# Kernel optimization log

Measured on AMD Instinct MI355X. Metric: run time of the kernel, lower is better.

Reference implementation:

```python
import jax, jax.numpy as jnp
import numpy as np
import math

H, SQK, SV, PQK, PV = 12, 16, 16, 4, 8
C1, C2 = 384, 128
B, N = 1, 768


def _rand_rot(key, shape):
    # random proper rotation matrices via QR of gaussian matrices
    m = jax.random.normal(key, shape + (3, 3), dtype=jnp.float32)
    q, r = jnp.linalg.qr(m)
    d = jnp.sign(jnp.diagonal(r, axis1=-2, axis2=-1))
    return q * d[..., None, :]


def setup_inputs() -> dict:
    key = jax.random.key(0)
    ks = jax.random.split(key, 16)
    s = 0.05
    return {
        'act': jax.random.normal(ks[0], (B, N, C1), dtype=jnp.float32),
        'act_2d': jax.random.normal(ks[1], (B, N, N, C2), dtype=jnp.float32),
        'sequence_mask': jnp.ones((B, N, 1), dtype=jnp.float32),
        'rot': _rand_rot(ks[2], (B, N)),
        'trans': jax.random.normal(ks[3], (B, N, 3), dtype=jnp.float32),
        'wq': jax.random.normal(ks[4], (C1, H * SQK), dtype=jnp.float32) * s,
        'wk': jax.random.normal(ks[5], (C1, H * SQK), dtype=jnp.float32) * s,
        'wv': jax.random.normal(ks[6], (C1, H * SV), dtype=jnp.float32) * s,
        'wqp': jax.random.normal(ks[7], (C1, H * PQK * 3), dtype=jnp.float32) * s,
        'bqp': jnp.zeros((H * PQK * 3,), dtype=jnp.float32),
        'wkp': jax.random.normal(ks[8], (C1, H * PQK * 3), dtype=jnp.float32) * s,
        'bkp': jnp.zeros((H * PQK * 3,), dtype=jnp.float32),
        'wvp': jax.random.normal(ks[9], (C1, H * PV * 3), dtype=jnp.float32) * s,
        'bvp': jnp.zeros((H * PV * 3,), dtype=jnp.float32),
        'w2d': jax.random.normal(ks[10], (C2, H), dtype=jnp.float32) * s,
        'b2d': jnp.zeros((H,), dtype=jnp.float32),
        'wfin': jax.random.normal(ks[11], (H * (C2 + SV + 4 * PV), C1), dtype=jnp.float32) * s,
        'bfin': jnp.zeros((C1,), dtype=jnp.float32),
        'tw': jnp.zeros((H,), dtype=jnp.float32),
    }


def _points(act, w, b, P):
    # torch: view [...,H,P*3] -> split into 3 chunks of P -> stack last => layout [H,3,P]
    p = (act @ w + b).reshape(*act.shape[:-1], H, 3, P)
    p = jnp.moveaxis(p, -2, -1)  # [B,N,H,P,3]
    return p.reshape(*act.shape[:-1], H * P, 3)


def _ipa(act, act_2d, sequence_mask, rot, trans,
         wq, wk, wv, wqp, bqp, wkp, bkp, wvp, bvp, w2d, b2d, wfin, bfin, tw):
    b, n, _ = act.shape
    q = (act @ wq).reshape(b, n, H, SQK) * math.sqrt(1.0 / SQK)
    k = (act @ wk).reshape(b, n, H, SQK)
    v = (act @ wv).reshape(b, n, H, SV)

    apply = lambda p: jnp.einsum('bnij,bnpj->bnpi', rot, p) + trans[:, :, None, :]
    qp = apply(_points(act, wqp, bqp, PQK))  # [B,N,H*PQK,3]
    kp = apply(_points(act, wkp, bkp, PQK))
    vp = apply(_points(act, wvp, bvp, PV))   # [B,N,H*PV,3]

    # point-distance logits
    pw = math.sqrt(2.0 / (9.0 * PQK)) * jax.nn.softplus(tw)  # [H]
    d2 = jnp.sum(jnp.square(qp[:, :, None] - kp[:, None]), -1)  # [B,N,N,H*PQK]
    d2 = d2.reshape(b, n, n, H, PQK).sum(-1)                    # [B,N,N,H]
    logits = -0.5 * pw * d2
    logits = logits + jnp.einsum('bqhc,bkhc->bqkh', q, k)
    logits = logits + act_2d @ w2d + b2d
    mask_2d = sequence_mask * jnp.swapaxes(sequence_mask, -1, -2)  # [B,N,N]
    logits = logits - 1e5 * (1.0 - mask_2d)[..., None]
    logits = logits * math.sqrt(1.0 / 3.0)
    attn = jax.nn.softmax(logits, axis=-2)  # over key residues

    res_scalar = jnp.einsum('bqkh,bkhc->bqhc', attn, v).reshape(b, n, H * SV)
    vp5 = vp.reshape(b, n, H, PV, 3)
    rpg = jnp.einsum('bqkh,bkhpd->bqhpd', attn, vp5).reshape(b, n, H * PV, 3)
    rpl = jnp.einsum('bnji,bnpj->bnpi', rot, rpg - trans[:, :, None, :])  # invert_apply
    norms = jnp.linalg.norm(rpl, axis=-1)
    r2d = jnp.einsum('bijh,bijc->bihc', attn, act_2d).reshape(b, n, H * C2)
    final = jnp.concatenate(
        [res_scalar, rpl[..., 0], rpl[..., 1], rpl[..., 2], norms, r2d], axis=-1)
    return final @ wfin + bfin


def reference(act, act_2d, sequence_mask, rot, trans,
              wq, wk, wv, wqp, bqp, wkp, bkp, wvp, bvp, w2d, b2d, wfin, bfin, tw):
    return _ipa(act, act_2d, sequence_mask, rot, trans,
                wq, wk, wv, wqp, bqp, wkp, bkp, wvp, bvp, w2d, b2d, wfin, bfin, tw)
```

## Files before the change

kernel.cpp:

```cpp
#include <hip/hip_runtime.h>
#include <math.h>

#define NH    12
#define NRES  768
#define C1V   384
#define C2V   128
#define NPROJ 1152
#define QKD   28
#define FDIM  2112
#define VVD   480
#define APAD  772
#define KSPLIT 11

typedef __attribute__((ext_vector_type(8))) short bf16x8;
typedef __attribute__((ext_vector_type(4))) float f32x4;

__device__ __forceinline__ float softplusf_(float x) {
    return (x > 20.f) ? x : log1pf(__expf(x));
}
__device__ __forceinline__ ushort f2bf(float x) {
    union { float f; unsigned u; } v; v.f = x;
    unsigned r = (v.u + 0x7fffu + ((v.u >> 16) & 1u)) >> 16;
    return (ushort)r;
}

__global__ __launch_bounds__(256) void kW_prep(
    const float* __restrict__ w2d, ushort* __restrict__ w2dT)
{
    int idx = blockIdx.x * 256 + threadIdx.x;
    int h = idx >> 7, c = idx & 127;
    w2dT[idx] = (h < NH) ? f2bf(w2d[c * NH + h]) : (ushort)0;
}

__global__ __launch_bounds__(256) void k1_proj(
    const float* __restrict__ act,
    const float* __restrict__ wq, const float* __restrict__ wk,
    const float* __restrict__ wv, const float* __restrict__ wqp,
    const float* __restrict__ wkp, const float* __restrict__ wvp,
    const float* __restrict__ bqp, const float* __restrict__ bkp,
    const float* __restrict__ bvp, float* __restrict__ proj)
{
    __shared__ float As[64 * 33];
    __shared__ float Bs[32 * 65];
    const int n0 = blockIdx.x * 64, m0 = blockIdx.y * 64;
    const int tid = threadIdx.x;
    const int tx = tid & 15, ty = tid >> 4;
    float c[4][4] = {};

    for (int kt = 0; kt < C1V; kt += 32) {
        for (int idx = tid; idx < 64 * 32; idx += 256) {
            int r = idx >> 5, j = idx & 31;
            As[r * 33 + j] = act[(m0 + r) * C1V + kt + j];
        }
        for (int idx = tid; idx < 32 * 64; idx += 256) {
            int r = idx >> 6, col = idx & 63;
            int jj = n0 + col, k = kt + r;
            float w;
            if      (jj < 192) w = wq [k * 192 + jj];
            else if (jj < 384) w = wk [k * 192 + jj - 192];
            else if (jj < 576) w = wv [k * 192 + jj - 384];
            else if (jj < 720) w = wqp[k * 144 + jj - 576];
            else if (jj < 864) w = wkp[k * 144 + jj - 720];
            else               w = wvp[k * 288 + jj - 864];
            Bs[r * 65 + col] = w;
        }
        __syncthreads();
        #pragma unroll
        for (int kk = 0; kk < 32; ++kk) {
            float a[4], b[4];
            #pragma unroll
            for (int i = 0; i < 4; ++i) a[i] = As[(ty * 4 + i) * 33 + kk];
            #pragma unroll
            for (int j = 0; j < 4; ++j) b[j] = Bs[kk * 65 + tx * 4 + j];
            #pragma unroll
            for (int i = 0; i < 4; ++i)
                #pragma unroll
                for (int j = 0; j < 4; ++j) c[i][j] += a[i] * b[j];
        }
        __syncthreads();
    }
    float biasv[4];
    #pragma unroll
    for (int j = 0; j < 4; ++j) {
        int col = n0 + tx * 4 + j;
        biasv[j] = (col >= 864) ? bvp[col - 864]
                 : (col >= 720) ? bkp[col - 720]
                 : (col >= 576) ? bqp[col - 576] : 0.f;
    }
    #pragma unroll
    for (int i = 0; i < 4; ++i) {
        float4 v;
        v.x = c[i][0] + biasv[0]; v.y = c[i][1] + biasv[1];
        v.z = c[i][2] + biasv[2]; v.w = c[i][3] + biasv[3];
        *(float4*)&proj[(m0 + ty * 4 + i) * NPROJ + n0 + tx * 4] = v;
    }
}

__global__ __launch_bounds__(64) void k2_prep(
    const float* __restrict__ proj, const float* __restrict__ rot,
    const float* __restrict__ trans, const float* __restrict__ tw,
    float* __restrict__ Qv, float* __restrict__ Kv,
    float* __restrict__ akArr, float* __restrict__ vv)
{
    const int n = blockIdx.x, tid = threadIdx.x;
    __shared__ float kp2[48];
    const float* pr = proj + n * NPROJ;
    float R[9], T[3];
    #pragma unroll
    for (int i = 0; i < 9; ++i) R[i] = rot[n * 9 + i];
    #pragma unroll
    for (int i = 0; i < 3; ++i) T[i] = trans[n * 3 + i];

    for (int idx = tid; idx < 192; idx += 64) {
        int h = idx >> 4, cc = idx & 15;
        Qv[(n * NH + h) * QKD + cc] = pr[idx] * 0.25f;
        Kv[(n * NH + h) * QKD + cc] = pr[192 + idx];
        vv[n * VVD + idx] = pr[384 + idx];
    }
    if (tid < 48) {
        int h = tid >> 2, p = tid & 3;
        float pwh = 0.23570226039551584f * softplusf_(tw[h]);
        float lx = pr[576 + h * 12 + p];
        float ly = pr[576 + h * 12 + 4 + p];
        float lz = pr[576 + h * 12 + 8 + p];
        float gx = R[0] * lx + R[1] * ly + R[2] * lz + T[0];
        float gy = R[3] * lx + R[4] * ly + R[5] * lz + T[1];
        float gz = R[6] * lx + R[7] * ly + R[8] * lz + T[2];
        float* qd = &Qv[(n * NH + h) * QKD + 16];
        qd[p] = pwh * gx; qd[4 + p] = pwh * gy; qd[8 + p] = pwh * gz;
        lx = pr[720 + h * 12 + p];
        ly = pr[720 + h * 12 + 4 + p];
        lz = pr[720 + h * 12 + 8 + p];
        gx = R[0] * lx + R[1] * ly + R[2] * lz + T[0];
        gy = R[3] * lx + R[4] * ly + R[5] * lz + T[1];
        gz = R[6] * lx + R[7] * ly + R[8] * lz + T[2];
        float* kd = &Kv[(n * NH + h) * QKD + 16];
        kd[p] = gx; kd[4 + p] = gy; kd[8 + p] = gz;
        kp2[tid] = gx * gx + gy * gy + gz * gz;
    }
    __syncthreads();
    if (tid < NH) {
        float pwh = 0.23570226039551584f * softplusf_(tw[tid]);
        akArr[n * NH + tid] = -0.5f * pwh *
            (kp2[tid * 4] + kp2[tid * 4 + 1] + kp2[tid * 4 + 2] + kp2[tid * 4 + 3]);
    }
    for (int idx = tid; idx < 96; idx += 64) {
        int h = idx >> 3, p = idx & 7;
        float lx = pr[864 + h * 24 + p];
        float ly = pr[864 + h * 24 + 8 + p];
        float lz = pr[864 + h * 24 + 16 + p];
        float gx = R[0] * lx + R[1] * ly + R[2] * lz + T[0];
        float gy = R[3] * lx + R[4] * ly + R[5] * lz + T[1];
        float gz = R[6] * lx + R[7] * ly + R[8] * lz + T[2];
        float* dst = &vv[n * VVD + 192 + h * 24 + p * 3];
        dst[0] = gx; dst[1] = gy; dst[2] = gz;
    }
}

__global__ __launch_bounds__(256) void k2b_qk(
    const float* __restrict__ Qv, const float* __restrict__ Kv,
    const float* __restrict__ akArr, float* __restrict__ qkBuf)
{
    const int h = blockIdx.z;
    const int k0 = blockIdx.x * 64, q0 = blockIdx.y * 64;
    __shared__ float As[64 * 29];
    __shared__ float Bs[64 * 29];
    const int tid = threadIdx.x, tx = tid & 15, ty = tid >> 4;

    for (int idx = tid; idx < 64 * 28; idx += 256) {
        int r = idx / 28, j = idx - r * 28;
        As[r * 29 + j] = Qv[((q0 + r) * NH + h) * QKD + j];
        Bs[r * 29 + j] = Kv[((k0 + r) * NH + h) * QKD + j];
    }
    __syncthreads();
    float c[4][4] = {};
    #pragma unroll
    for (int kk = 0; kk < 28; ++kk) {
        float a[4], b[4];
        #pragma unroll
        for (int i = 0; i < 4; ++i) a[i] = As[(ty * 4 + i) * 29 + kk];
        #pragma unroll
        for (int j = 0; j < 4; ++j) b[j] = Bs[(tx * 4 + j) * 29 + kk];
        #pragma unroll
        for (int i = 0; i < 4; ++i)
            #pragma unroll
            for (int j = 0; j < 4; ++j) c[i][j] += a[i] * b[j];
    }
    float akv[4];
    #pragma unroll
    for (int j = 0; j < 4; ++j) akv[j] = akArr[(k0 + tx * 4 + j) * NH + h];
    #pragma unroll
    for (int i = 0; i < 4; ++i) {
        float4 v;
        v.x = c[i][0] + akv[0]; v.y = c[i][1] + akv[1];
        v.z = c[i][2] + akv[2]; v.w = c[i][3] + akv[3];
        *(float4*)&qkBuf[((q0 + ty * 4 + i) * NH + h) * NRES + k0 + tx * 4] = v;
    }
}

__global__ __launch_bounds__(256) void kA_mfma(
    const float* __restrict__ act2d, const float* __restrict__ smask,
    const ushort* __restrict__ w2dT, float* __restrict__ qkBuf)
{
    const int q = blockIdx.y, k0 = blockIdx.x * 64, tid = threadIdx.x;
    __shared__ ushort tile[64 * 136];
    const int lane = tid & 63, wv = tid >> 6;
    const int nb = lane & 15, quad = lane >> 4;

    bf16x8 bfr[4];
    #pragma unroll
    for (int s = 0; s < 4; ++s)
        bfr[s] = *(const bf16x8*)&w2dT[nb * 128 + quad * 8 + s * 32];

    const float* src = act2d + ((size_t)q * NRES + k0) * C2V;
    #pragma unroll
    for (int i = 0; i < 8; ++i) {
        int f = tid + i * 256;
        int r = f >> 5, c4 = f & 31;
        float4 v = ((const float4*)src)[f];
        ushort4 o = { f2bf(v.x), f2bf(v.y), f2bf(v.z), f2bf(v.w) };
        *(ushort4*)&tile[r * 136 + c4 * 4] = o;
    }
    __syncthreads();

    f32x4 acc = {0.f, 0.f, 0.f, 0.f};
    #pragma unroll
    for (int s = 0; s < 4; ++s) {
        bf16x8 af = *(const bf16x8*)&tile[(wv * 16 + nb) * 136 + quad * 8 + s * 32];
        acc = __builtin_amdgcn_mfma_f32_16x16x32_bf16(af, bfr[s], acc, 0, 0, 0);
    }

    if (nb < NH) {
        const int kb = k0 + wv * 16 + quad * 4;
        float* dst = &qkBuf[((size_t)(q * NH + nb)) * NRES + kb];
        float4 old = *(float4*)dst;
        float4 sm = *(const float4*)&smask[kb];
        const float smq = smask[q];
        const float scale = 0.5773502691896258f;
        float4 outv;
        outv.x = (old.x + acc[0] - 1e5f * (1.f - smq * sm.x)) * scale;
        outv.y = (old.y + acc[1] - 1e5f * (1.f - smq * sm.y)) * scale;
        outv.z = (old.z + acc[2] - 1e5f * (1.f - smq * sm.z)) * scale;
        outv.w = (old.w + acc[3] - 1e5f * (1.f - smq * sm.w)) * scale;
        *(float4*)dst = outv;
    }
}

__global__ __launch_bounds__(256) void kC_attn(
    const float* __restrict__ act2d, const float* __restrict__ qkBuf,
    const float* __restrict__ vv, const float* __restrict__ rot,
    const float* __restrict__ trans, float* __restrict__ F)
{
    const int q = blockIdx.x, tid = threadIdx.x;
    __shared__ float attnS[NH * APAD];
    __shared__ float scr[1536];
    __shared__ float red[NH * 4];
    __shared__ float mh[NH], lh[NH];
    __shared__ float rotS[9], transS[3];

    if (tid < 9) rotS[tid] = rot[q * 9 + tid];
    if (tid < 3) transS[tid] = trans[q * 3 + tid];

    float lg[3][NH];
    #pragma unroll
    for (int h = 0; h < NH; ++h)
        #pragma unroll
        for (int i = 0; i < 3; ++i)
            lg[i][h] = qkBuf[((size_t)(q * NH + h)) * NRES + tid + 256 * i];

    const int wv_ = tid >> 6, lane = tid & 63;
    #pragma unroll
    for (int h = 0; h < NH; ++h) {
        float v = fmaxf(fmaxf(lg[0][h], lg[1][h]), lg[2][h]);
        for (int off = 32; off > 0; off >>= 1) v = fmaxf(v, __shfl_down(v, off, 64));
        if (lane == 0) red[h * 4 + wv_] = v;
    }
    __syncthreads();
    if (tid < NH)
        mh[tid] = fmaxf(fmaxf(red[tid * 4], red[tid * 4 + 1]),
                        fmaxf(red[tid * 4 + 2], red[tid * 4 + 3]));
    __syncthreads();
    float lsum[NH];
    #pragma unroll
    for (int h = 0; h < NH; ++h) lsum[h] = 0.f;
    #pragma unroll
    for (int i = 0; i < 3; ++i)
        #pragma unroll
        for (int h = 0; h < NH; ++h) {
            float e = __expf(lg[i][h] - mh[h]);
            attnS[h * APAD + tid + 256 * i] = e;
            lsum[h] += e;
        }
    #pragma unroll
    for (int h = 0; h < NH; ++h) {
        float v = lsum[h];
        for (int off = 32; off > 0; off >>= 1) v += __shfl_down(v, off, 64);
        if (lane == 0) red[h * 4 + wv_] = v;
    }
    __syncthreads();
    if (tid < NH)
        lh[tid] = 1.f / (red[tid * 4] + red[tid * 4 + 1] + red[tid * 4 + 2] + red[tid * 4 + 3]);
    __syncthreads();

    const int cq = tid & 31, hg = (tid >> 5) & 3, kg = tid >> 7;
    const int h0 = 3 * hg;
    const float* abase = act2d + ((size_t)q * NRES + kg * 384) * C2V + cq * 4;
    const float* at0 = &attnS[(h0    ) * APAD + kg * 384];
    const float* at1 = &attnS[(h0 + 1) * APAD + kg * 384];
    const float* at2 = &attnS[(h0 + 2) * APAD + kg * 384];
    float4 a0 = {0,0,0,0}, a1 = {0,0,0,0}, a2 = {0,0,0,0};

    for (int kk = 0; kk < 384; kk += 4) {
        float4 t0 = *(const float4*)&abase[(size_t)(kk    ) * C2V];
        float4 t1 = *(const float4*)&abase[(size_t)(kk + 1) * C2V];
        float4 t2 = *(const float4*)&abase[(size_t)(kk + 2) * C2V];
        float4 t3 = *(const float4*)&abase[(size_t)(kk + 3) * C2V];
        float4 p0 = *(const float4*)&at0[kk];
        float4 p1 = *(const float4*)&at1[kk];
        float4 p2 = *(const float4*)&at2[kk];
        a0.x += p0.x*t0.x + p0.y*t1.x + p0.z*t2.x + p0.w*t3.x;
        a0.y += p0.x*t0.y + p0.y*t1.y + p0.z*t2.y + p0.w*t3.y;
        a0.z += p0.x*t0.z + p0.y*t1.z + p0.z*t2.z + p0.w*t3.z;
        a0.w += p0.x*t0.w + p0.y*t1.w + p0.z*t2.w + p0.w*t3.w;
        a1.x += p1.x*t0.x + p1.y*t1.x + p1.z*t2.x + p1.w*t3.x;
        a1.y += p1.x*t0.y + p1.y*t1.y + p1.z*t2.y + p1.w*t3.y;
        a1.z += p1.x*t0.z + p1.y*t1.z + p1.z*t2.z + p1.w*t3.z;
        a1.w += p1.x*t0.w + p1.y*t1.w + p1.z*t2.w + p1.w*t3.w;
        a2.x += p2.x*t0.x + p2.y*t1.x + p2.z*t2.x + p2.w*t3.x;
        a2.y += p2.x*t0.y + p2.y*t1.y + p2.z*t2.y + p2.w*t3.y;
        a2.z += p2.x*t0.z + p2.y*t1.z + p2.z*t2.z + p2.w*t3.z;
        a2.w += p2.x*t0.w + p2.y*t1.w + p2.z*t2.w + p2.w*t3.w;
    }
    if (kg == 1) {
        *(float4*)&scr[(h0    ) * 128 + cq * 4] = a0;
        *(float4*)&scr[(h0 + 1) * 128 + cq * 4] = a1;
        *(float4*)&scr[(h0 + 2) * 128 + cq * 4] = a2;
    }
    __syncthreads();
    float* Fq = F + q * FDIM;
    if (kg == 0) {
        float4 b0 = *(const float4*)&scr[(h0    ) * 128 + cq * 4];
        float4 b1 = *(const float4*)&scr[(h0 + 1) * 128 + cq * 4];
        float4 b2 = *(const float4*)&scr[(h0 + 2) * 128 + cq * 4];
        float l0 = lh[h0], l1 = lh[h0 + 1], l2 = lh[h0 + 2];
        float4 o0 = {(a0.x+b0.x)*l0, (a0.y+b0.y)*l0, (a0.z+b0.z)*l0, (a0.w+b0.w)*l0};
        float4 o1 = {(a1.x+b1.x)*l1, (a1.y+b1.y)*l1, (a1.z+b1.z)*l1, (a1.w+b1.w)*l1};
        float4 o2 = {(a2.x+b2.x)*l2, (a2.y+b2.y)*l2, (a2.z+b2.z)*l2, (a2.w+b2.w)*l2};
        *(float4*)&Fq[576 + (h0    ) * 128 + cq * 4] = o0;
        *(float4*)&Fq[576 + (h0 + 1) * 128 + cq * 4] = o1;
        *(float4*)&Fq[576 + (h0 + 2) * 128 + cq * 4] = o2;
    }
    __syncthreads();

    const int j4 = tid & 127;
    const int kgv = tid >> 7;
    float p0 = 0.f, p1 = 0.f, p2 = 0.f, p3 = 0.f;
    if (j4 < 120) {
        const int h = (j4 < 48) ? (j4 >> 2) : ((j4 - 48) / 6);
        const float* at = &attnS[h * APAD + kgv * 384];
        const float* col = vv + (size_t)(kgv * 384) * VVD + j4 * 4;
        #pragma unroll 4
        for (int k = 0; k < 384; ++k) {
            float a = at[k];
            float4 v = *(const float4*)(col + (size_t)k * VVD);
            p0 += a * v.x; p1 += a * v.y; p2 += a * v.z; p3 += a * v.w;
        }
    }
    __syncthreads();
    if (j4 < 120) {
        float4 pv = {p0, p1, p2, p3};
        *(float4*)&scr[(kgv * 120 + j4) * 4] = pv;
    }
    __syncthreads();
    if (tid < 120) {
        float4 a = *(const float4*)&scr[tid * 4];
        float4 b = *(const float4*)&scr[(120 + tid) * 4];
        const int h = (tid < 48) ? (tid >> 2) : ((tid - 48) / 6);
        const float il = lh[h];
        float4 s = {(a.x + b.x) * il, (a.y + b.y) * il,
                    (a.z + b.z) * il, (a.w + b.w) * il};
        if (tid < 48) {
            *(float4*)&Fq[tid * 4] = s;
        } else {
            *(float4*)&scr[1024 + (tid - 48) * 4] = s;
        }
    }
    __syncthreads();
    if (tid < 96) {
        float gx = scr[1024 + tid * 3]     - transS[0];
        float gy = scr[1024 + tid * 3 + 1] - transS[1];
        float gz = scr[1024 + tid * 3 + 2] - transS[2];
        float x = rotS[0] * gx + rotS[3] * gy + rotS[6] * gz;
        float y = rotS[1] * gx + rotS[4] * gy + rotS[7] * gz;
        float z = rotS[2] * gx + rotS[5] * gy + rotS[8] * gz;
        Fq[192 + tid] = x;
        Fq[288 + tid] = y;
        Fq[384 + tid] = z;
        Fq[480 + tid] = sqrtf(x * x + y * y + z * z);
    }
}

__global__ __launch_bounds__(256) void k5_partial(
    const float* __restrict__ F, const float* __restrict__ wfin,
    float* __restrict__ part)
{
    const int n0 = blockIdx.x * 64, m0 = blockIdx.y * 64, kz = blockIdx.z;
    const int kbeg = kz * 192;
    __shared__ float As[64 * 33];
    __shared__ float Bs[32 * 65];
    const int tid = threadIdx.x, tx = tid & 15, ty = tid >> 4;
    float c[4][4] = {};

    for (int kt = kbeg; kt < kbeg + 192; kt += 32) {
        for (int idx = tid; idx < 64 * 32; idx += 256) {
            int r = idx >> 5, j = idx & 31;
            As[r * 33 + j] = F[(m0 + r) * FDIM + kt + j];
        }
        for (int idx = tid; idx < 32 * 64; idx += 256) {
            int r = idx >> 6, col = idx & 63;
            Bs[r * 65 + col] = wfin[(kt + r) * 384 + n0 + col];
        }
        __syncthreads();
        #pragma unroll
        for (int kk = 0; kk < 32; ++kk) {
            float a[4], b[4];
            #pragma unroll
            for (int i = 0; i < 4; ++i) a[i] = As[(ty * 4 + i) * 33 + kk];
            #pragma unroll
            for (int j = 0; j < 4; ++j) b[j] = Bs[kk * 65 + tx * 4 + j];
            #pragma unroll
            for (int i = 0; i < 4; ++i)
                #pragma unroll
                for (int j = 0; j < 4; ++j) c[i][j] += a[i] * b[j];
        }
        __syncthreads();
    }
    float* dst = part + (size_t)kz * (768 * 384);
    #pragma unroll
    for (int i = 0; i < 4; ++i) {
        float4 v = {c[i][0], c[i][1], c[i][2], c[i][3]};
        *(float4*)&dst[(m0 + ty * 4 + i) * 384 + n0 + tx * 4] = v;
    }
}

__global__ __launch_bounds__(256) void k5_reduce(
    const float* __restrict__ part, const float* __restrict__ bfin,
    float* __restrict__ out)
{
    const int e = blockIdx.x * 256 + threadIdx.x;
    const float4* p = (const float4*)part;
    float4 b = ((const float4*)bfin)[e % 96];
    float4 s = {b.x, b.y, b.z, b.w};
    #pragma unroll
    for (int kz = 0; kz < KSPLIT; ++kz) {
        float4 v = p[(size_t)kz * 73728 + e];
        s.x += v.x; s.y += v.y; s.z += v.z; s.w += v.w;
    }
    ((float4*)out)[e] = s;
}

extern "C" void kernel_launch(void* const* d_in, const int* in_sizes, int n_in,
                              void* d_out, int out_size, void* d_ws, size_t ws_size,
                              hipStream_t stream) {
    const float* act   = (const float*)d_in[0];
    const float* act2d = (const float*)d_in[1];
    const float* smask = (const float*)d_in[2];
    const float* rot   = (const float*)d_in[3];
    const float* trans = (const float*)d_in[4];
    const float* wq    = (const float*)d_in[5];
    const float* wk    = (const float*)d_in[6];
    const float* wvv   = (const float*)d_in[7];
    const float* wqp   = (const float*)d_in[8];
    const float* bqp   = (const float*)d_in[9];
    const float* wkp   = (const float*)d_in[10];
    const float* bkp   = (const float*)d_in[11];
    const float* wvp   = (const float*)d_in[12];
    const float* bvp   = (const float*)d_in[13];
    const float* w2d   = (const float*)d_in[14];
    const float* wfin  = (const float*)d_in[16];
    const float* bfin  = (const float*)d_in[17];
    const float* tw    = (const float*)d_in[18];

    float* W     = (float*)d_ws;
    float* proj  = W;
    float* Qv    = proj  + 768 * NPROJ;
    float* Kv    = Qv    + 768 * NH * QKD;
    float* akArr = Kv    + 768 * NH * QKD;
    float* vvA   = akArr + 768 * NH;
    float* qkBuf = vvA   + 768 * VVD;
    float* F     = qkBuf + 768 * NH * NRES;
    ushort* w2dT = (ushort*)(F + 768 * FDIM);
    float* part  = qkBuf;

    kW_prep<<<dim3(8), 256, 0, stream>>>(w2d, w2dT);
    k1_proj<<<dim3(18, 12), 256, 0, stream>>>(act, wq, wk, wvv, wqp, wkp, wvp,
                                              bqp, bkp, bvp, proj);
    k2_prep<<<dim3(NRES), 64, 0, stream>>>(proj, rot, trans, tw, Qv, Kv, akArr, vvA);
    k2b_qk<<<dim3(12, 12, NH), 256, 0, stream>>>(Qv, Kv, akArr, qkBuf);
    kA_mfma<<<dim3(12, NRES), 256, 0, stream>>>(act2d, smask, w2dT, qkBuf);
    kC_attn<<<dim3(NRES), 256, 0, stream>>>(act2d, qkBuf, vvA, rot, trans, F);
    k5_partial<<<dim3(6, 12, KSPLIT), 256, 0, stream>>>(F, wfin, part);
    k5_reduce<<<dim3(288), 256, 0, stream>>>(part, bfin, (float*)d_out);
}
```

Before: 687.2 us.

## Fuse pair-bias MFMA and attention into one online-softmax kernel

Merges the kernel that computes the act_2d pair-bias logits with the attention kernel, using a flash-style online softmax over 64-key chunks. The goal is to stop reading the 300MB act_2d tensor twice and to avoid the qkBuf read-modify-write round trip. Each chunk's act_2d tile is loaded for the MFMA and then read again, likely from cache, for the weighted sum. The cost is one block per query with many barriers per chunk, so the kernel has much less parallelism than the 12x768 grid it replaces.

```diff
diff --git a/kernel.cpp b/kernel.cpp
--- a/kernel.cpp
+++ b/kernel.cpp
@@ -9,7 +9,6 @@
 #define QKD   28
 #define FDIM  2112
 #define VVD   480
-#define APAD  772
 #define KSPLIT 11
 
 typedef __attribute__((ext_vector_type(8))) short bf16x8;
@@ -198,139 +197,148 @@
     }
 }
 
-__global__ __launch_bounds__(256) void kA_mfma(
-    const float* __restrict__ act2d, const float* __restrict__ smask,
-    const ushort* __restrict__ w2dT, float* __restrict__ qkBuf)
-{
-    const int q = blockIdx.y, k0 = blockIdx.x * 64, tid = threadIdx.x;
+__global__ __launch_bounds__(256) void kF_fused(
+    const float* __restrict__ act2d, const float* __restrict__ qkBuf,
+    const float* __restrict__ smask, const ushort* __restrict__ w2dT,
+    const float* __restrict__ vv, const float* __restrict__ rot,
+    const float* __restrict__ trans, float* __restrict__ F)
+{
+    const int q = blockIdx.x, tid = threadIdx.x;
     __shared__ ushort tile[64 * 136];
-    const int lane = tid & 63, wv = tid >> 6;
+    __shared__ float p_lds[16 * 72];
+    __shared__ float redM[64], redS[64];
+    __shared__ float mS[16], sS[16], fS[16];
+    __shared__ float scr[1536];
+    __shared__ float rotS[9], transS[3];
+
+    const int lane = tid & 63, wvI = tid >> 6;
     const int nb = lane & 15, quad = lane >> 4;
+    const int cq = tid & 31, hg = (tid >> 5) & 3, kg = tid >> 7;
+    const int h0 = 3 * hg;
+    const int j4 = tid & 127, kgv = tid >> 7;
+    const int hv = (j4 < 48) ? (j4 >> 2) : ((j4 - 48) / 6);
 
     bf16x8 bfr[4];
     #pragma unroll
     for (int s = 0; s < 4; ++s)
         bfr[s] = *(const bf16x8*)&w2dT[nb * 128 + quad * 8 + s * 32];
 
-    const float* src = act2d + ((size_t)q * NRES + k0) * C2V;
-    #pragma unroll
-    for (int i = 0; i < 8; ++i) {
-        int f = tid + i * 256;
-        int r = f >> 5, c4 = f & 31;
-        float4 v = ((const float4*)src)[f];
-        ushort4 o = { f2bf(v.x), f2bf(v.y), f2bf(v.z), f2bf(v.w) };
-        *(ushort4*)&tile[r * 136 + c4 * 4] = o;
-    }
-    __syncthreads();
-
-    f32x4 acc = {0.f, 0.f, 0.f, 0.f};
-    #pragma unroll
-    for (int s = 0; s < 4; ++s) {
-        bf16x8 af = *(const bf16x8*)&tile[(wv * 16 + nb) * 136 + quad * 8 + s * 32];
-        acc = __builtin_amdgcn_mfma_f32_16x16x32_bf16(af, bfr[s], acc, 0, 0, 0);
-    }
-
-    if (nb < NH) {
-        const int kb = k0 + wv * 16 + quad * 4;
-        float* dst = &qkBuf[((size_t)(q * NH + nb)) * NRES + kb];
-        float4 old = *(float4*)dst;
-        float4 sm = *(const float4*)&smask[kb];
-        const float smq = smask[q];
-        const float scale = 0.5773502691896258f;
-        float4 outv;
-        outv.x = (old.x + acc[0] - 1e5f * (1.f - smq * sm.x)) * scale;
-        outv.y = (old.y + acc[1] - 1e5f * (1.f - smq * sm.y)) * scale;
-        outv.z = (old.z + acc[2] - 1e5f * (1.f - smq * sm.z)) * scale;
-        outv.w = (old.w + acc[3] - 1e5f * (1.f - smq * sm.w)) * scale;
-        *(float4*)dst = outv;
-    }
-}
-
-__global__ __launch_bounds__(256) void kC_attn(
-    const float* __restrict__ act2d, const float* __restrict__ qkBuf,
-    const float* __restrict__ vv, const float* __restrict__ rot,
-    const float* __restrict__ trans, float* __restrict__ F)
-{
-    const int q = blockIdx.x, tid = threadIdx.x;
-    __shared__ float attnS[NH * APAD];
-    __shared__ float scr[1536];
-    __shared__ float red[NH * 4];
-    __shared__ float mh[NH], lh[NH];
-    __shared__ float rotS[9], transS[3];
-
+    if (tid < 16) { mS[tid] = -1e30f; sS[tid] = 0.f; fS[tid] = 0.f; }
     if (tid < 9) rotS[tid] = rot[q * 9 + tid];
     if (tid < 3) transS[tid] = trans[q * 3 + tid];
-
-    float lg[3][NH];
-    #pragma unroll
-    for (int h = 0; h < NH; ++h)
-        #pragma unroll
-        for (int i = 0; i < 3; ++i)
-            lg[i][h] = qkBuf[((size_t)(q * NH + h)) * NRES + tid + 256 * i];
-
-    const int wv_ = tid >> 6, lane = tid & 63;
-    #pragma unroll
-    for (int h = 0; h < NH; ++h) {
-        float v = fmaxf(fmaxf(lg[0][h], lg[1][h]), lg[2][h]);
-        for (int off = 32; off > 0; off >>= 1) v = fmaxf(v, __shfl_down(v, off, 64));
-        if (lane == 0) red[h * 4 + wv_] = v;
-    }
-    __syncthreads();
-    if (tid < NH)
-        mh[tid] = fmaxf(fmaxf(red[tid * 4], red[tid * 4 + 1]),
-                        fmaxf(red[tid * 4 + 2], red[tid * 4 + 3]));
-    __syncthreads();
-    float lsum[NH];
-    #pragma unroll
-    for (int h = 0; h < NH; ++h) lsum[h] = 0.f;
-    #pragma unroll
-    for (int i = 0; i < 3; ++i)
-        #pragma unroll
-        for (int h = 0; h < NH; ++h) {
-            float e = __expf(lg[i][h] - mh[h]);
-            attnS[h * APAD + tid + 256 * i] = e;
-            lsum[h] += e;
-        }
-    #pragma unroll
-    for (int h = 0; h < NH; ++h) {
-        float v = lsum[h];
-        for (int off = 32; off > 0; off >>= 1) v += __shfl_down(v, off, 64);
-        if (lane == 0) red[h * 4 + wv_] = v;
-    }
-    __syncthreads();
-    if (tid < NH)
-        lh[tid] = 1.f / (red[tid * 4] + red[tid * 4 + 1] + red[tid * 4 + 2] + red[tid * 4 + 3]);
-    __syncthreads();
-
-    const int cq = tid & 31, hg = (tid >> 5) & 3, kg = tid >> 7;
-    const int h0 = 3 * hg;
-    const float* abase = act2d + ((size_t)q * NRES + kg * 384) * C2V + cq * 4;
-    const float* at0 = &attnS[(h0    ) * APAD + kg * 384];
-    const float* at1 = &attnS[(h0 + 1) * APAD + kg * 384];
-    const float* at2 = &attnS[(h0 + 2) * APAD + kg * 384];
+    const float smq = smask[q];
+
     float4 a0 = {0,0,0,0}, a1 = {0,0,0,0}, a2 = {0,0,0,0};
-
-    for (int kk = 0; kk < 384; kk += 4) {
-        float4 t0 = *(const float4*)&abase[(size_t)(kk    ) * C2V];
-        float4 t1 = *(const float4*)&abase[(size_t)(kk + 1) * C2V];
-        float4 t2 = *(const float4*)&abase[(size_t)(kk + 2) * C2V];
-        float4 t3 = *(const float4*)&abase[(size_t)(kk + 3) * C2V];
-        float4 p0 = *(const float4*)&at0[kk];
-        float4 p1 = *(const float4*)&at1[kk];
-        float4 p2 = *(const float4*)&at2[kk];
-        a0.x += p0.x*t0.x + p0.y*t1.x + p0.z*t2.x + p0.w*t3.x;
-        a0.y += p0.x*t0.y + p0.y*t1.y + p0.z*t2.y + p0.w*t3.y;
-        a0.z += p0.x*t0.z + p0.y*t1.z + p0.z*t2.z + p0.w*t3.z;
-        a0.w += p0.x*t0.w + p0.y*t1.w + p0.z*t2.w + p0.w*t3.w;
-        a1.x += p1.x*t0.x + p1.y*t1.x + p1.z*t2.x + p1.w*t3.x;
-        a1.y += p1.x*t0.y + p1.y*t1.y + p1.z*t2.y + p1.w*t3.y;
-        a1.z += p1.x*t0.z + p1.y*t1.z + p1.z*t2.z + p1.w*t3.z;
-        a1.w += p1.x*t0.w + p1.y*t1.w + p1.z*t2.w + p1.w*t3.w;
-        a2.x += p2.x*t0.x + p2.y*t1.x + p2.z*t2.x + p2.w*t3.x;
-        a2.y += p2.x*t0.y + p2.y*t1.y + p2.z*t2.y + p2.w*t3.y;
-        a2.z += p2.x*t0.z + p2.y*t1.z + p2.z*t2.z + p2.w*t3.z;
-        a2.w += p2.x*t0.w + p2.y*t1.w + p2.z*t2.w + p2.w*t3.w;
-    }
+    float v0 = 0.f, v1 = 0.f, v2 = 0.f, v3 = 0.f;
+
+    for (int kc = 0; kc < 12; ++kc) {
+        const int kbase = kc * 64;
+        const float* src = act2d + ((size_t)q * NRES + kbase) * C2V;
+        #pragma unroll
+        for (int i = 0; i < 8; ++i) {
+            int f = tid + i * 256;
+            int r = f >> 5, c4 = f & 31;
+            float4 v = ((const float4*)src)[f];
+            ushort4 o = { f2bf(v.x), f2bf(v.y), f2bf(v.z), f2bf(v.w) };
+            *(ushort4*)&tile[r * 136 + c4 * 4] = o;
+        }
+        const int kb = kbase + wvI * 16 + quad * 4;
+        float4 qk = {0,0,0,0}, mk = {1.f,1.f,1.f,1.f};
+        if (nb < NH) {
+            qk = *(const float4*)&qkBuf[((size_t)(q * NH + nb)) * NRES + kb];
+            mk = *(const float4*)&smask[kb];
+        }
+        __syncthreads();
+        f32x4 acc = {0.f, 0.f, 0.f, 0.f};
+        #pragma unroll
+        for (int s = 0; s < 4; ++s) {
+            bf16x8 af = *(const bf16x8*)&tile[(wvI * 16 + nb) * 136 + quad * 8 + s * 32];
+            acc = __builtin_amdgcn_mfma_f32_16x16x32_bf16(af, bfr[s], acc, 0, 0, 0);
+        }
+        float l0 = -1e30f, l1 = -1e30f, l2 = -1e30f, l3 = -1e30f;
+        if (nb < NH) {
+            const float scale = 0.5773502691896258f;
+            l0 = (qk.x + acc[0] - 1e5f * (1.f - smq * mk.x)) * scale;
+            l1 = (qk.y + acc[1] - 1e5f * (1.f - smq * mk.y)) * scale;
+            l2 = (qk.z + acc[2] - 1e5f * (1.f - smq * mk.z)) * scale;
+            l3 = (qk.w + acc[3] - 1e5f * (1.f - smq * mk.w)) * scale;
+        }
+        float lmax = fmaxf(fmaxf(l0, l1), fmaxf(l2, l3));
+        lmax = fmaxf(lmax, __shfl_xor(lmax, 16, 64));
+        lmax = fmaxf(lmax, __shfl_xor(lmax, 32, 64));
+        if (quad == 0) redM[nb * 4 + wvI] = lmax;
+        __syncthreads();
+        if (tid < NH) {
+            float cm = fmaxf(fmaxf(redM[tid * 4], redM[tid * 4 + 1]),
+                             fmaxf(redM[tid * 4 + 2], redM[tid * 4 + 3]));
+            float mo = mS[tid], mn = fmaxf(mo, cm);
+            fS[tid] = __expf(mo - mn);
+            mS[tid] = mn;
+        }
+        __syncthreads();
+        float psum = 0.f;
+        if (nb < NH) {
+            float mn = mS[nb];
+            float e0 = __expf(l0 - mn), e1 = __expf(l1 - mn);
+            float e2 = __expf(l2 - mn), e3 = __expf(l3 - mn);
+            psum = e0 + e1 + e2 + e3;
+            float4 ev = {e0, e1, e2, e3};
+            *(float4*)&p_lds[nb * 72 + wvI * 16 + quad * 4] = ev;
+        }
+        psum += __shfl_xor(psum, 16, 64);
+        psum += __shfl_xor(psum, 32, 64);
+        if (quad == 0) redS[nb * 4 + wvI] = psum;
+        __syncthreads();
+        if (tid < NH)
+            sS[tid] = sS[tid] * fS[tid] + redS[tid * 4] + redS[tid * 4 + 1]
+                                        + redS[tid * 4 + 2] + redS[tid * 4 + 3];
+        {
+            float f0 = fS[h0], f1 = fS[h0 + 1], f2 = fS[h0 + 2];
+            a0.x *= f0; a0.y *= f0; a0.z *= f0; a0.w *= f0;
+            a1.x *= f1; a1.y *= f1; a1.z *= f1; a1.w *= f1;
+            a2.x *= f2; a2.y *= f2; a2.z *= f2; a2.w *= f2;
+            const float* ab = act2d + ((size_t)q * NRES + kbase + kg * 32) * C2V + cq * 4;
+            const float* p0r = &p_lds[(h0    ) * 72 + kg * 32];
+            const float* p1r = &p_lds[(h0 + 1) * 72 + kg * 32];
+            const float* p2r = &p_lds[(h0 + 2) * 72 + kg * 32];
+            for (int kk = 0; kk < 32; kk += 4) {
+                float4 t0 = *(const float4*)&ab[(size_t)(kk    ) * C2V];
+                float4 t1 = *(const float4*)&ab[(size_t)(kk + 1) * C2V];
+                float4 t2 = *(const float4*)&ab[(size_t)(kk + 2) * C2V];
+                float4 t3 = *(const float4*)&ab[(size_t)(kk + 3) * C2V];
+                float4 pp0 = *(const float4*)&p0r[kk];
+                float4 pp1 = *(const float4*)&p1r[kk];
+                float4 pp2 = *(const float4*)&p2r[kk];
+                a0.x += pp0.x*t0.x + pp0.y*t1.x + pp0.z*t2.x + pp0.w*t3.x;
+                a0.y += pp0.x*t0.y + pp0.y*t1.y + pp0.z*t2.y + pp0.w*t3.y;
+                a0.z += pp0.x*t0.z + pp0.y*t1.z + pp0.z*t2.z + pp0.w*t3.z;
+                a0.w += pp0.x*t0.w + pp0.y*t1.w + pp0.z*t2.w + pp0.w*t3.w;
+                a1.x += pp1.x*t0.x + pp1.y*t1.x + pp1.z*t2.x + pp1.w*t3.x;
+                a1.y += pp1.x*t0.y + pp1.y*t1.y + pp1.z*t2.y + pp1.w*t3.y;
+                a1.z += pp1.x*t0.z + pp1.y*t1.z + pp1.z*t2.z + pp1.w*t3.z;
+                a1.w += pp1.x*t0.w + pp1.y*t1.w + pp1.z*t2.w + pp1.w*t3.w;
+                a2.x += pp2.x*t0.x + pp2.y*t1.x + pp2.z*t2.x + pp2.w*t3.x;
+                a2.y += pp2.x*t0.y + pp2.y*t1.y + pp2.z*t2.y + pp2.w*t3.y;
+                a2.z += pp2.x*t0.z + pp2.y*t1.z + pp2.z*t2.z + pp2.w*t3.z;
+                a2.w += pp2.x*t0.w + pp2.y*t1.w + pp2.z*t2.w + pp2.w*t3.w;
+            }
+            if (j4 < 120) {
+                float fv = fS[hv];
+                v0 *= fv; v1 *= fv; v2 *= fv; v3 *= fv;
+                const float* pk  = &p_lds[hv * 72 + kgv * 32];
+                const float* col = vv + (size_t)(kbase + kgv * 32) * VVD + j4 * 4;
+                #pragma unroll 4
+                for (int k = 0; k < 32; ++k) {
+                    float a = pk[k];
+                    float4 t = *(const float4*)(col + (size_t)k * VVD);
+                    v0 += a * t.x; v1 += a * t.y; v2 += a * t.z; v3 += a * t.w;
+                }
+            }
+        }
+        __syncthreads();
+    }
+
+    float i0 = 1.f / sS[h0], i1 = 1.f / sS[h0 + 1], i2 = 1.f / sS[h0 + 2];
     if (kg == 1) {
         *(float4*)&scr[(h0    ) * 128 + cq * 4] = a0;
         *(float4*)&scr[(h0 + 1) * 128 + cq * 4] = a1;
@@ -342,33 +350,16 @@
         float4 b0 = *(const float4*)&scr[(h0    ) * 128 + cq * 4];
         float4 b1 = *(const float4*)&scr[(h0 + 1) * 128 + cq * 4];
         float4 b2 = *(const float4*)&scr[(h0 + 2) * 128 + cq * 4];
-        float l0 = lh[h0], l1 = lh[h0 + 1], l2 = lh[h0 + 2];
-        float4 o0 = {(a0.x+b0.x)*l0, (a0.y+b0.y)*l0, (a0.z+b0.z)*l0, (a0.w+b0.w)*l0};
-        float4 o1 = {(a1.x+b1.x)*l1, (a1.y+b1.y)*l1, (a1.z+b1.z)*l1, (a1.w+b1.w)*l1};
-        float4 o2 = {(a2.x+b2.x)*l2, (a2.y+b2.y)*l2, (a2.z+b2.z)*l2, (a2.w+b2.w)*l2};
+        float4 o0 = {(a0.x+b0.x)*i0, (a0.y+b0.y)*i0, (a0.z+b0.z)*i0, (a0.w+b0.w)*i0};
+        float4 o1 = {(a1.x+b1.x)*i1, (a1.y+b1.y)*i1, (a1.z+b1.z)*i1, (a1.w+b1.w)*i1};
+        float4 o2 = {(a2.x+b2.x)*i2, (a2.y+b2.y)*i2, (a2.z+b2.z)*i2, (a2.w+b2.w)*i2};
         *(float4*)&Fq[576 + (h0    ) * 128 + cq * 4] = o0;
         *(float4*)&Fq[576 + (h0 + 1) * 128 + cq * 4] = o1;
         *(float4*)&Fq[576 + (h0 + 2) * 128 + cq * 4] = o2;
     }
     __syncthreads();
-
-    const int j4 = tid & 127;
-    const int kgv = tid >> 7;
-    float p0 = 0.f, p1 = 0.f, p2 = 0.f, p3 = 0.f;
     if (j4 < 120) {
-        const int h = (j4 < 48) ? (j4 >> 2) : ((j4 - 48) / 6);
-        const float* at = &attnS[h * APAD + kgv * 384];
-        const float* col = vv + (size_t)(kgv * 384) * VVD + j4 * 4;
-        #pragma unroll 4
-        for (int k = 0; k < 384; ++k) {
-            float a = at[k];
-            float4 v = *(const float4*)(col + (size_t)k * VVD);
-            p0 += a * v.x; p1 += a * v.y; p2 += a * v.z; p3 += a * v.w;
-        }
-    }
-    __syncthreads();
-    if (j4 < 120) {
-        float4 pv = {p0, p1, p2, p3};
+        float4 pv = {v0, v1, v2, v3};
         *(float4*)&scr[(kgv * 120 + j4) * 4] = pv;
     }
     __syncthreads();
@@ -376,7 +367,7 @@
         float4 a = *(const float4*)&scr[tid * 4];
         float4 b = *(const float4*)&scr[(120 + tid) * 4];
         const int h = (tid < 48) ? (tid >> 2) : ((tid - 48) / 6);
-        const float il = lh[h];
+        const float il = 1.f / sS[h];
         float4 s = {(a.x + b.x) * il, (a.y + b.y) * il,
                     (a.z + b.z) * il, (a.w + b.w) * il};
         if (tid < 48) {
@@ -497,8 +488,8 @@
                                               bqp, bkp, bvp, proj);
     k2_prep<<<dim3(NRES), 64, 0, stream>>>(proj, rot, trans, tw, Qv, Kv, akArr, vvA);
     k2b_qk<<<dim3(12, 12, NH), 256, 0, stream>>>(Qv, Kv, akArr, qkBuf);
-    kA_mfma<<<dim3(12, NRES), 256, 0, stream>>>(act2d, smask, w2dT, qkBuf);
-    kC_attn<<<dim3(NRES), 256, 0, stream>>>(act2d, qkBuf, vvA, rot, trans, F);
+    kF_fused<<<dim3(NRES), 256, 0, stream>>>(act2d, qkBuf, smask, w2dT, vvA,
+                                             rot, trans, F);
     k5_partial<<<dim3(6, 12, KSPLIT), 256, 0, stream>>>(F, wfin, part);
     k5_reduce<<<dim3(288), 256, 0, stream>>>(part, bfin, (float*)d_out);
 }
```

Result: slower. 916.1 us (+33.3%).
